# Optimization experiments

Hardware: AMD Instinct MI355X
Metric: run time of the kernel (lower is better)

The kernel has to match this reference:

```python
import jax, jax.numpy as jnp
import numpy as np

N_NODES = 100000
N_EDGES = 1600000
D_IN = 128
D_HID = 64


def setup_inputs() -> dict:
    key = jax.random.key(0)
    k1, k2, k3, k4 = jax.random.split(key, 4)
    x = jax.random.normal(k1, (N_NODES, D_IN), dtype=jnp.float32)
    edge_index = jax.random.randint(k2, (2, N_EDGES), 0, N_NODES, dtype=jnp.int64)
    W1 = jax.random.normal(k3, (D_IN, D_HID), dtype=jnp.float32) / np.sqrt(D_IN)
    b1 = jnp.zeros((D_HID,), dtype=jnp.float32)
    W2 = jax.random.normal(k4, (D_HID, 1), dtype=jnp.float32) / np.sqrt(D_HID)
    b2 = jnp.zeros((1,), dtype=jnp.float32)
    return {"x": x, "edge_index": edge_index, "W1": W1, "b1": b1, "W2": W2, "b2": b2}


def _gcn_layer(x, W, b, src, dst, norm, n):
    # PyG GCNConv: linear transform, then normalized scatter-add aggregation, then bias
    h = x @ W                                   # [N, d_out]
    msg = h[src] * norm[:, None]                # gather + edge-weight   [E', d_out]
    out = jax.ops.segment_sum(msg, dst, num_segments=n)  # scatter-add
    return out + b


def reference(x, edge_index, W1, b1, W2, b2):
    n = x.shape[0]
    loops = jnp.arange(n, dtype=edge_index.dtype)
    src = jnp.concatenate([edge_index[0], loops])  # self-loops added (GCN default)
    dst = jnp.concatenate([edge_index[1], loops])
    # symmetric normalization: deg^{-1/2}[src] * deg^{-1/2}[dst]
    deg = jax.ops.segment_sum(jnp.ones(dst.shape, x.dtype), dst, num_segments=n)
    dis = jnp.where(deg > 0, jax.lax.rsqrt(jnp.maximum(deg, 1e-12)), 0.0)
    norm = dis[src] * dis[dst]
    h = jax.nn.relu(_gcn_layer(x, W1, b1, src, dst, norm, n))
    y = _gcn_layer(h, W2, b2, src, dst, norm, n)   # [N, 1]
    # ConstantPad1d((0, num_node_features-1), 0) -> [N, D_IN]
    return jnp.pad(y, ((0, 0), (0, x.shape[1] - 1)))
```

## Files before the change

### kernel.cpp

```cpp
#include <hip/hip_runtime.h>

#define N_NODES 100000
#define N_EDGES 1600000
#define D_IN 128
#define D_HID 64

#define BKT_SHIFT 8
#define BKT_NODES 256
#define NB 391
#define NBLK 392
#define SLOT 32
#define SEG4 (SLOT / 4)
#define REG4 (NBLK * SEG4)
#define BKT_CAP 5120
#define OVF_CAP 8192

#define FST 512
#define BST 1024
#define GEMM_NB 782

typedef __attribute__((ext_vector_type(8))) short bf16x8;
typedef __attribute__((ext_vector_type(4))) float f32x4;

__device__ __forceinline__ unsigned short f2b(float f) {
    union { float f; unsigned u; } c; c.f = f;
    unsigned r = (c.u + 0x7FFFu + ((c.u >> 16) & 1u)) >> 16;
    return (unsigned short)r;
}
__device__ __forceinline__ float blo(unsigned u) { return __uint_as_float(u << 16); }
__device__ __forceinline__ float bhi(unsigned u) { return __uint_as_float(u & 0xffff0000u); }

#define LS 136
__global__ __launch_bounds__(FST) void k_fused(const int* __restrict__ src,
                                               const int* __restrict__ dst,
                                               int* __restrict__ pairs,
                                               int* __restrict__ cnt_blk,
                                               int* __restrict__ ovf_cnt,
                                               int2* __restrict__ ovf, int E,
                                               const float* __restrict__ x,
                                               const float* __restrict__ W1,
                                               unsigned short* __restrict__ h1s, int n) {
    __shared__ __align__(16) unsigned char smem[52224];
    int tid = threadIdx.x;

    if (blockIdx.x < NBLK) {
        int* lp   = (int*)smem;
        int* lcur = lp + NB * SLOT;
        for (int t = tid; t < NB; t += FST) lcur[t] = 0;
        __syncthreads();
        int chunk = (E + NBLK - 1) / NBLK;
        int beg = blockIdx.x * chunk;
        int end = min(beg + chunk, E);
        for (int e = beg + tid; e < end; e += FST) {
            int d = dst[e], s = src[e];
            int bk = d >> BKT_SHIFT;
            int slot = atomicAdd(&lcur[bk], 1);
            if (slot < SLOT)
                lp[(bk << 5) + slot] = (s << BKT_SHIFT) | (d & (BKT_NODES - 1));
            else {
                int o = atomicAdd(ovf_cnt, 1);
                if (o < OVF_CAP) ovf[o] = make_int2(s, d);
            }
        }
        __syncthreads();
        uint4* p4 = (uint4*)pairs;
        const uint4* lp4 = (const uint4*)lp;
        for (int i4 = tid; i4 < NB * SEG4; i4 += FST) {
            int bk = i4 >> 3;
            int c = min(lcur[bk], SLOT);
            if (((i4 & 7) << 2) < c)
                p4[((size_t)bk * NBLK + blockIdx.x) * SEG4 + (i4 & 7)] = lp4[i4];
        }
        for (int t = tid; t < NB; t += FST)
            cnt_blk[t * NBLK + blockIdx.x] = min(lcur[t], SLOT);
    } else {
        unsigned short* ws = (unsigned short*)smem;
        unsigned short* xs = ws + 64 * LS;
        int half = tid >> 8;
        int t2 = tid & 255;
        int node0 = (blockIdx.x - NBLK) * 128 + half * 64;
        unsigned short* xsh = xs + half * 64 * LS;

#pragma unroll
        for (int it = 0; it < 16; ++it) {
            int e = tid + it * 512;
            int k = e >> 6, f = e & 63;
            ws[f * LS + k] = f2b(W1[e]);
        }
#pragma unroll
        for (int it = 0; it < 8; ++it) {
            int e4 = t2 + it * 256;
            int node = e4 >> 5;
            int k = (e4 & 31) * 4;
            float4 v = make_float4(0.f, 0.f, 0.f, 0.f);
            if (node0 + node < n)
                v = ((const float4*)x)[((size_t)(node0 + node) * D_IN + k) >> 2];
            uint2 u;
            u.x = (unsigned)f2b(v.x) | ((unsigned)f2b(v.y) << 16);
            u.y = (unsigned)f2b(v.z) | ((unsigned)f2b(v.w) << 16);
            *(uint2*)&xsh[node * LS + k] = u;
        }
        __syncthreads();

        int wv = t2 >> 6;
        int lane = t2 & 63;
        int m16 = lane & 15;
        int q = lane >> 4;

        bf16x8 afrag[4];
#pragma unroll
        for (int ks = 0; ks < 4; ++ks)
            afrag[ks] = *(const bf16x8*)&xsh[(wv * 16 + m16) * LS + ks * 32 + q * 8];

        f32x4 acc[4];
#pragma unroll
        for (int ft = 0; ft < 4; ++ft) acc[ft] = (f32x4){0.f, 0.f, 0.f, 0.f};

#pragma unroll
        for (int ft = 0; ft < 4; ++ft)
#pragma unroll
            for (int ks = 0; ks < 4; ++ks) {
                bf16x8 bfrag = *(const bf16x8*)&ws[(ft * 16 + m16) * LS + ks * 32 + q * 8];
                acc[ft] = __builtin_amdgcn_mfma_f32_16x16x32_bf16(afrag[ks], bfrag, acc[ft], 0, 0, 0);
            }

#pragma unroll
        for (int r = 0; r < 4; ++r) {
            int node = node0 + wv * 16 + q * 4 + r;
            if (node < n) {
#pragma unroll
                for (int ft = 0; ft < 4; ++ft)
                    h1s[(size_t)node * D_HID + ft * 16 + m16] = f2b(acc[ft][r]);
            }
        }
    }
}

__global__ __launch_bounds__(BST) void k_bsort(const uint4* __restrict__ pairs4,
                                               const int* __restrict__ cnt_blk,
                                               const int* __restrict__ ovf_cnt,
                                               const int2* __restrict__ ovf,
                                               int* __restrict__ srcs_sorted,
                                               int* __restrict__ row_start,
                                               int* __restrict__ row_end,
                                               float* __restrict__ dis, int n) {
    __shared__ uint4 reg4[REG4];
    __shared__ int segc[NBLK];
    __shared__ int cnt[BKT_NODES];
    __shared__ int exc[BKT_NODES];
    __shared__ int sorted[BKT_CAP];
    __shared__ int nE_sh;
    int b = blockIdx.x;
    int tid = threadIdx.x;
    int node0 = b << BKT_SHIFT;
    int ocnt = min(ovf_cnt[0], OVF_CAP);
    const uint4* region = pairs4 + (size_t)b * REG4;

    for (int i = tid; i < NBLK; i += BST) segc[i] = cnt_blk[b * NBLK + i];
    if (tid < BKT_NODES) cnt[tid] = 0;
    __syncthreads();

    for (int i4 = tid; i4 < REG4; i4 += BST) {
        int c = segc[i4 >> 3];
        int k = (i4 & 7) * 4;
        if (k < c) {
            uint4 v = region[i4];
            reg4[i4] = v;
            atomicAdd(&cnt[v.x & (BKT_NODES - 1)], 1);
            if (k + 1 < c) atomicAdd(&cnt[v.y & (BKT_NODES - 1)], 1);
            if (k + 2 < c) atomicAdd(&cnt[v.z & (BKT_NODES - 1)], 1);
            if (k + 3 < c) atomicAdd(&cnt[v.w & (BKT_NODES - 1)], 1);
        }
    }
    for (int k = tid; k < ocnt; k += BST) {
        int2 e = ovf[k];
        if ((e.y >> BKT_SHIFT) == b) atomicAdd(&cnt[e.y & (BKT_NODES - 1)], 1);
    }
    __syncthreads();

    if (tid < 64) {
        int run = 0;
        for (int c = 0; c < BKT_NODES; c += 64) {
            int v = cnt[c + tid];
            int inc = v;
            for (int off = 1; off < 64; off <<= 1) {
                int t2 = __shfl_up(inc, off);
                if (tid >= off) inc += t2;
            }
            exc[c + tid] = run + inc - v;
            run += __shfl(inc, 63);
        }
        if (tid == 63) nE_sh = run;
    }
    __syncthreads();

    if (tid < BKT_NODES) {
        int node = node0 + tid;
        if (node < n) {
            int rs = b * BKT_CAP + exc[tid];
            row_start[node] = rs;
            row_end[node] = rs + cnt[tid];
            dis[node] = rsqrtf((float)cnt[tid] + 1.0f);
        }
    }
    int nE = nE_sh;
    __syncthreads();
    if (tid < BKT_NODES) cnt[tid] = exc[tid];
    __syncthreads();

    for (int i4 = tid; i4 < REG4; i4 += BST) {
        int c = segc[i4 >> 3];
        int k = (i4 & 7) * 4;
        if (k < c) {
            uint4 v = reg4[i4];
            { int p = atomicAdd(&cnt[v.x & (BKT_NODES - 1)], 1); sorted[p] = (int)(v.x >> 8); }
            if (k + 1 < c) { int p = atomicAdd(&cnt[v.y & (BKT_NODES - 1)], 1); sorted[p] = (int)(v.y >> 8); }
            if (k + 2 < c) { int p = atomicAdd(&cnt[v.z & (BKT_NODES - 1)], 1); sorted[p] = (int)(v.z >> 8); }
            if (k + 3 < c) { int p = atomicAdd(&cnt[v.w & (BKT_NODES - 1)], 1); sorted[p] = (int)(v.w >> 8); }
        }
    }
    for (int k = tid; k < ocnt; k += BST) {
        int2 e = ovf[k];
        if ((e.y >> BKT_SHIFT) == b) {
            int p = atomicAdd(&cnt[e.y & (BKT_NODES - 1)], 1);
            sorted[p] = e.x;
        }
    }
    __syncthreads();

    int gbase = b * BKT_CAP;
    for (int k = tid; k < nE; k += BST)
        srcs_sorted[gbase + k] = sorted[k];
}

__global__ __launch_bounds__(256) void k_gather1(const int* __restrict__ srcs,
                                                 const int* __restrict__ row_start,
                                                 const int* __restrict__ row_end,
                                                 const float* __restrict__ dis,
                                                 const uint4* __restrict__ h4,
                                                 const float* __restrict__ b1,
                                                 const float* __restrict__ W2,
                                                 float* __restrict__ zd, int n) {
    int i = blockIdx.x * 8 + (threadIdx.x >> 5);
    int lane = threadIdx.x & 63;
    int g = (lane >> 3) & 3;
    int m8 = lane & 7;
    float dd = dis[i];

    float a0, a1, a2, a3, a4, a5, a6, a7;
    {
        uint4 u = h4[(unsigned)i * 8u + m8];
        float w = (g == 0) ? dd : 0.f;
        a0 = w * blo(u.x); a1 = w * bhi(u.x);
        a2 = w * blo(u.y); a3 = w * bhi(u.y);
        a4 = w * blo(u.z); a5 = w * bhi(u.z);
        a6 = w * blo(u.w); a7 = w * bhi(u.w);
    }

#define ACC(u, ds) { a0 = fmaf(ds, blo(u.x), a0); a1 = fmaf(ds, bhi(u.x), a1); \
                     a2 = fmaf(ds, blo(u.y), a2); a3 = fmaf(ds, bhi(u.y), a3); \
                     a4 = fmaf(ds, blo(u.z), a4); a5 = fmaf(ds, bhi(u.z), a5); \
                     a6 = fmaf(ds, blo(u.w), a6); a7 = fmaf(ds, bhi(u.w), a7); }
    int end = row_end[i];
    int j = row_start[i] + g;
    for (; j + 12 < end; j += 16) {
        int s0 = srcs[j];
        int s1 = srcs[j + 4];
        int s2 = srcs[j + 8];
        int s3 = srcs[j + 12];
        float d0 = dis[s0], d1 = dis[s1], d2 = dis[s2], d3 = dis[s3];
        uint4 u0 = h4[(unsigned)s0 * 8u + m8];
        uint4 u1 = h4[(unsigned)s1 * 8u + m8];
        uint4 u2 = h4[(unsigned)s2 * 8u + m8];
        uint4 u3 = h4[(unsigned)s3 * 8u + m8];
        ACC(u0, d0); ACC(u1, d1); ACC(u2, d2); ACC(u3, d3);
    }
    for (; j + 4 < end; j += 8) {
        int s0 = srcs[j];
        int s1 = srcs[j + 4];
        float d0 = dis[s0], d1 = dis[s1];
        uint4 u0 = h4[(unsigned)s0 * 8u + m8];
        uint4 u1 = h4[(unsigned)s1 * 8u + m8];
        ACC(u0, d0); ACC(u1, d1);
    }
    if (j < end) {
        int s0 = srcs[j];
        float d0 = dis[s0];
        uint4 u0 = h4[(unsigned)s0 * 8u + m8];
        ACC(u0, d0);
    }
#undef ACC

#pragma unroll
    for (int off = 8; off < 32; off <<= 1) {
        a0 += __shfl_xor(a0, off); a1 += __shfl_xor(a1, off);
        a2 += __shfl_xor(a2, off); a3 += __shfl_xor(a3, off);
        a4 += __shfl_xor(a4, off); a5 += __shfl_xor(a5, off);
        a6 += __shfl_xor(a6, off); a7 += __shfl_xor(a7, off);
    }
    float4 ba = ((const float4*)b1)[m8 * 2];
    float4 bb = ((const float4*)b1)[m8 * 2 + 1];
    float4 wa = ((const float4*)W2)[m8 * 2];
    float4 wb = ((const float4*)W2)[m8 * 2 + 1];
    float v = fmaxf(fmaf(dd, a0, ba.x), 0.f) * wa.x + fmaxf(fmaf(dd, a1, ba.y), 0.f) * wa.y
            + fmaxf(fmaf(dd, a2, ba.z), 0.f) * wa.z + fmaxf(fmaf(dd, a3, ba.w), 0.f) * wa.w
            + fmaxf(fmaf(dd, a4, bb.x), 0.f) * wb.x + fmaxf(fmaf(dd, a5, bb.y), 0.f) * wb.y
            + fmaxf(fmaf(dd, a6, bb.z), 0.f) * wb.z + fmaxf(fmaf(dd, a7, bb.w), 0.f) * wb.w;
#pragma unroll
    for (int off = 1; off < 8; off <<= 1) v += __shfl_xor(v, off);
    if ((lane & 31) == 0) zd[i] = v * dd;
}

__global__ __launch_bounds__(256) void k_gather2(const int* __restrict__ srcs,
                                                 const int* __restrict__ row_start,
                                                 const int* __restrict__ row_end,
                                                 const float* __restrict__ dis,
                                                 const float* __restrict__ zd,
                                                 const float* __restrict__ b2,
                                                 float* __restrict__ out, int n) {
    int i = blockIdx.x * 8 + (threadIdx.x >> 5);
    int l = threadIdx.x & 31;
    float acc = 0.f;
    int beg = row_start[i], end = row_end[i];
    for (int j = beg + l; j < end; j += 32)
        acc += zd[srcs[j]];
#pragma unroll
    for (int off = 1; off < 32; off <<= 1) acc += __shfl_xor(acc, off);
    float y = (acc + zd[i]) * dis[i] + b2[0];
    float4 v = make_float4(0.f, 0.f, 0.f, 0.f);
    if (l == 0) v.x = y;
    ((float4*)out)[(size_t)i * 32 + l] = v;
}

extern "C" void kernel_launch(void* const* d_in, const int* in_sizes, int n_in,
                              void* d_out, int out_size, void* d_ws, size_t ws_size,
                              hipStream_t stream) {
    const float* x  = (const float*)d_in[0];
    const int*   ei = (const int*)d_in[1];
    const float* W1 = (const float*)d_in[2];
    const float* b1 = (const float*)d_in[3];
    const float* W2 = (const float*)d_in[4];
    const float* b2 = (const float*)d_in[5];
    float* out = (float*)d_out;

    const int n = N_NODES;
    const int E = N_EDGES;
    const int* src = ei;
    const int* dst = ei + E;

    int* pairs       = (int*)d_ws;
    int* cnt_blk     = pairs + (size_t)NB * NBLK * SLOT;
    int* srcs_sorted = cnt_blk + (size_t)NB * NBLK;
    int* row_start   = srcs_sorted + (size_t)NB * BKT_CAP;
    int* row_end     = row_start + n;
    int* ovf_cnt     = row_end + n;
    int2* ovf        = (int2*)(ovf_cnt + 4);
    float* dis       = (float*)(ovf + OVF_CAP);
    unsigned short* h1s = (unsigned short*)(dis + n);
    float* zd        = (float*)(h1s + (size_t)n * D_HID);

    hipMemsetAsync(ovf_cnt, 0, sizeof(int), stream);
    k_fused<<<NBLK + GEMM_NB, FST, 0, stream>>>(src, dst, pairs, cnt_blk, ovf_cnt,
                                                ovf, E, x, W1, h1s, n);
    k_bsort<<<NB, BST, 0, stream>>>((const uint4*)pairs, cnt_blk, ovf_cnt, ovf,
                                    srcs_sorted, row_start, row_end, dis, n);
    k_gather1<<<(n + 7) / 8, 256, 0, stream>>>(srcs_sorted, row_start, row_end, dis,
                                               (const uint4*)h1s, b1, W2, zd, n);
    k_gather2<<<(n + 7) / 8, 256, 0, stream>>>(srcs_sorted, row_start, row_end, dis,
                                               zd, b2, out, n);
}
```

Before: 194.0 us.

## Replace two-pass bucket sort CSR build with atomic histogram and scatter

Replaces the per-block LDS bucketing plus per-bucket shared-memory counting sort with a global atomic degree histogram, a per-bucket prefix scan kernel producing row offsets and cursors, and a global-atomic scatter of source ids into CSR order. This removes the large intermediate pairs buffer and overflow path, but relies on millions of global atomics on random addresses and adds one more kernel launch. Edge order within a row becomes nondeterministic, which can change floating-point summation order.

```diff
diff --git a/kernel.cpp b/kernel.cpp
--- a/kernel.cpp
+++ b/kernel.cpp
@@ -8,16 +8,11 @@
 #define BKT_SHIFT 8
 #define BKT_NODES 256
 #define NB 391
-#define NBLK 392
-#define SLOT 32
-#define SEG4 (SLOT / 4)
-#define REG4 (NBLK * SEG4)
 #define BKT_CAP 5120
-#define OVF_CAP 8192
-
+
+#define HIST_NB 392
+#define GEMM_NB 782
 #define FST 512
-#define BST 1024
-#define GEMM_NB 782
 
 typedef __attribute__((ext_vector_type(8))) short bf16x8;
 typedef __attribute__((ext_vector_type(4))) float f32x4;
@@ -31,54 +26,24 @@
 __device__ __forceinline__ float bhi(unsigned u) { return __uint_as_float(u & 0xffff0000u); }
 
 #define LS 136
-__global__ __launch_bounds__(FST) void k_fused(const int* __restrict__ src,
-                                               const int* __restrict__ dst,
-                                               int* __restrict__ pairs,
-                                               int* __restrict__ cnt_blk,
-                                               int* __restrict__ ovf_cnt,
-                                               int2* __restrict__ ovf, int E,
+__global__ __launch_bounds__(FST) void k_fused(const int* __restrict__ dst,
+                                               int* __restrict__ deg, int E,
                                                const float* __restrict__ x,
                                                const float* __restrict__ W1,
                                                unsigned short* __restrict__ h1s, int n) {
     __shared__ __align__(16) unsigned char smem[52224];
     int tid = threadIdx.x;
 
-    if (blockIdx.x < NBLK) {
-        int* lp   = (int*)smem;
-        int* lcur = lp + NB * SLOT;
-        for (int t = tid; t < NB; t += FST) lcur[t] = 0;
-        __syncthreads();
-        int chunk = (E + NBLK - 1) / NBLK;
-        int beg = blockIdx.x * chunk;
-        int end = min(beg + chunk, E);
-        for (int e = beg + tid; e < end; e += FST) {
-            int d = dst[e], s = src[e];
-            int bk = d >> BKT_SHIFT;
-            int slot = atomicAdd(&lcur[bk], 1);
-            if (slot < SLOT)
-                lp[(bk << 5) + slot] = (s << BKT_SHIFT) | (d & (BKT_NODES - 1));
-            else {
-                int o = atomicAdd(ovf_cnt, 1);
-                if (o < OVF_CAP) ovf[o] = make_int2(s, d);
-            }
-        }
-        __syncthreads();
-        uint4* p4 = (uint4*)pairs;
-        const uint4* lp4 = (const uint4*)lp;
-        for (int i4 = tid; i4 < NB * SEG4; i4 += FST) {
-            int bk = i4 >> 3;
-            int c = min(lcur[bk], SLOT);
-            if (((i4 & 7) << 2) < c)
-                p4[((size_t)bk * NBLK + blockIdx.x) * SEG4 + (i4 & 7)] = lp4[i4];
-        }
-        for (int t = tid; t < NB; t += FST)
-            cnt_blk[t * NBLK + blockIdx.x] = min(lcur[t], SLOT);
+    if (blockIdx.x < HIST_NB) {
+        int stride = HIST_NB * FST;
+        for (int e = blockIdx.x * FST + tid; e < E; e += stride)
+            atomicAdd(&deg[dst[e]], 1);
     } else {
         unsigned short* ws = (unsigned short*)smem;
         unsigned short* xs = ws + 64 * LS;
         int half = tid >> 8;
         int t2 = tid & 255;
-        int node0 = (blockIdx.x - NBLK) * 128 + half * 64;
+        int node0 = (blockIdx.x - HIST_NB) * 128 + half * 64;
         unsigned short* xsh = xs + half * 64 * LS;
 
 #pragma unroll
@@ -136,46 +101,18 @@
     }
 }
 
-__global__ __launch_bounds__(BST) void k_bsort(const uint4* __restrict__ pairs4,
-                                               const int* __restrict__ cnt_blk,
-                                               const int* __restrict__ ovf_cnt,
-                                               const int2* __restrict__ ovf,
-                                               int* __restrict__ srcs_sorted,
-                                               int* __restrict__ row_start,
-                                               int* __restrict__ row_end,
-                                               float* __restrict__ dis, int n) {
-    __shared__ uint4 reg4[REG4];
-    __shared__ int segc[NBLK];
+__global__ __launch_bounds__(256) void k_rows(const int* __restrict__ deg,
+                                              int* __restrict__ row_start,
+                                              int* __restrict__ row_end,
+                                              int* __restrict__ cursor,
+                                              float* __restrict__ dis, int n) {
     __shared__ int cnt[BKT_NODES];
     __shared__ int exc[BKT_NODES];
-    __shared__ int sorted[BKT_CAP];
-    __shared__ int nE_sh;
     int b = blockIdx.x;
     int tid = threadIdx.x;
-    int node0 = b << BKT_SHIFT;
-    int ocnt = min(ovf_cnt[0], OVF_CAP);
-    const uint4* region = pairs4 + (size_t)b * REG4;
-
-    for (int i = tid; i < NBLK; i += BST) segc[i] = cnt_blk[b * NBLK + i];
-    if (tid < BKT_NODES) cnt[tid] = 0;
-    __syncthreads();
-
-    for (int i4 = tid; i4 < REG4; i4 += BST) {
-        int c = segc[i4 >> 3];
-        int k = (i4 & 7) * 4;
-        if (k < c) {
-            uint4 v = region[i4];
-            reg4[i4] = v;
-            atomicAdd(&cnt[v.x & (BKT_NODES - 1)], 1);
-            if (k + 1 < c) atomicAdd(&cnt[v.y & (BKT_NODES - 1)], 1);
-            if (k + 2 < c) atomicAdd(&cnt[v.z & (BKT_NODES - 1)], 1);
-            if (k + 3 < c) atomicAdd(&cnt[v.w & (BKT_NODES - 1)], 1);
-        }
-    }
-    for (int k = tid; k < ocnt; k += BST) {
-        int2 e = ovf[k];
-        if ((e.y >> BKT_SHIFT) == b) atomicAdd(&cnt[e.y & (BKT_NODES - 1)], 1);
-    }
+    int node = (b << BKT_SHIFT) + tid;
+    int d = (node < n) ? deg[node] : 0;
+    cnt[tid] = d;
     __syncthreads();
 
     if (tid < 64) {
@@ -190,47 +127,28 @@
             exc[c + tid] = run + inc - v;
             run += __shfl(inc, 63);
         }
-        if (tid == 63) nE_sh = run;
     }
     __syncthreads();
 
-    if (tid < BKT_NODES) {
-        int node = node0 + tid;
-        if (node < n) {
-            int rs = b * BKT_CAP + exc[tid];
-            row_start[node] = rs;
-            row_end[node] = rs + cnt[tid];
-            dis[node] = rsqrtf((float)cnt[tid] + 1.0f);
-        }
-    }
-    int nE = nE_sh;
-    __syncthreads();
-    if (tid < BKT_NODES) cnt[tid] = exc[tid];
-    __syncthreads();
-
-    for (int i4 = tid; i4 < REG4; i4 += BST) {
-        int c = segc[i4 >> 3];
-        int k = (i4 & 7) * 4;
-        if (k < c) {
-            uint4 v = reg4[i4];
-            { int p = atomicAdd(&cnt[v.x & (BKT_NODES - 1)], 1); sorted[p] = (int)(v.x >> 8); }
-            if (k + 1 < c) { int p = atomicAdd(&cnt[v.y & (BKT_NODES - 1)], 1); sorted[p] = (int)(v.y >> 8); }
-            if (k + 2 < c) { int p = atomicAdd(&cnt[v.z & (BKT_NODES - 1)], 1); sorted[p] = (int)(v.z >> 8); }
-            if (k + 3 < c) { int p = atomicAdd(&cnt[v.w & (BKT_NODES - 1)], 1); sorted[p] = (int)(v.w >> 8); }
-        }
-    }
-    for (int k = tid; k < ocnt; k += BST) {
-        int2 e = ovf[k];
-        if ((e.y >> BKT_SHIFT) == b) {
-            int p = atomicAdd(&cnt[e.y & (BKT_NODES - 1)], 1);
-            sorted[p] = e.x;
-        }
-    }
-    __syncthreads();
-
-    int gbase = b * BKT_CAP;
-    for (int k = tid; k < nE; k += BST)
-        srcs_sorted[gbase + k] = sorted[k];
+    if (node < n) {
+        int rs = b * BKT_CAP + exc[tid];
+        row_start[node] = rs;
+        row_end[node] = rs + d;
+        cursor[node] = rs;
+        dis[node] = rsqrtf((float)d + 1.0f);
+    }
+}
+
+__global__ __launch_bounds__(256) void k_scatter(const int* __restrict__ src,
+                                                 const int* __restrict__ dst,
+                                                 int* __restrict__ cursor,
+                                                 int* __restrict__ srcs_sorted, int E) {
+    int stride = gridDim.x * 256;
+    for (int e = blockIdx.x * 256 + threadIdx.x; e < E; e += stride) {
+        int d = dst[e], s = src[e];
+        int p = atomicAdd(&cursor[d], 1);
+        srcs_sorted[p] = s;
+    }
 }
 
 __global__ __launch_bounds__(256) void k_gather1(const int* __restrict__ srcs,
@@ -348,22 +266,19 @@
     const int* src = ei;
     const int* dst = ei + E;
 
-    int* pairs       = (int*)d_ws;
-    int* cnt_blk     = pairs + (size_t)NB * NBLK * SLOT;
-    int* srcs_sorted = cnt_blk + (size_t)NB * NBLK;
+    int* deg         = (int*)d_ws;
+    int* cursor      = deg + n;
+    int* srcs_sorted = cursor + n;
     int* row_start   = srcs_sorted + (size_t)NB * BKT_CAP;
     int* row_end     = row_start + n;
-    int* ovf_cnt     = row_end + n;
-    int2* ovf        = (int2*)(ovf_cnt + 4);
-    float* dis       = (float*)(ovf + OVF_CAP);
+    float* dis       = (float*)(row_end + n);
     unsigned short* h1s = (unsigned short*)(dis + n);
     float* zd        = (float*)(h1s + (size_t)n * D_HID);
 
-    hipMemsetAsync(ovf_cnt, 0, sizeof(int), stream);
-    k_fused<<<NBLK + GEMM_NB, FST, 0, stream>>>(src, dst, pairs, cnt_blk, ovf_cnt,
-                                                ovf, E, x, W1, h1s, n);
-    k_bsort<<<NB, BST, 0, stream>>>((const uint4*)pairs, cnt_blk, ovf_cnt, ovf,
-                                    srcs_sorted, row_start, row_end, dis, n);
+    hipMemsetAsync(deg, 0, n * sizeof(int), stream);
+    k_fused<<<HIST_NB + GEMM_NB, FST, 0, stream>>>(dst, deg, E, x, W1, h1s, n);
+    k_rows<<<NB, 256, 0, stream>>>(deg, row_start, row_end, cursor, dis, n);
+    k_scatter<<<1568, 256, 0, stream>>>(src, dst, cursor, srcs_sorted, E);
     k_gather1<<<(n + 7) / 8, 256, 0, stream>>>(srcs_sorted, row_start, row_end, dis,
                                                (const uint4*)h1s, b1, W2, zd, n);
     k_gather2<<<(n + 7) / 8, 256, 0, stream>>>(srcs_sorted, row_start, row_end, dis,
```

Measured after the change: 348.6 us. 1.8x slower.

## Quantize hidden features to int8 with per-node scales for gather

Applied to the files above, without the earlier changes.

The GEMM epilogue now quantizes each node's 64-wide hidden row to int8, using a per-node absmax scale. It stages the rows through shared memory for coalesced 16-byte stores. The sort kernel folds the degree normalization and the quantization scale into one per-node factor. The first gather then reads 8-byte int8 rows instead of 16-byte bf16 rows, which halves the random-gather traffic. In exchange it loses precision relative to bf16 and adds a shuffle reduction and a block sync in the GEMM epilogue.

```diff
diff --git a/kernel.cpp b/kernel.cpp
--- a/kernel.cpp
+++ b/kernel.cpp
@@ -39,7 +39,8 @@
                                                int2* __restrict__ ovf, int E,
                                                const float* __restrict__ x,
                                                const float* __restrict__ W1,
-                                               unsigned short* __restrict__ h1s, int n) {
+                                               unsigned char* __restrict__ h1s8,
+                                               float* __restrict__ scale, int n) {
     __shared__ __align__(16) unsigned char smem[52224];
     int tid = threadIdx.x;
 
@@ -124,14 +125,31 @@
                 acc[ft] = __builtin_amdgcn_mfma_f32_16x16x32_bf16(afrag[ks], bfrag, acc[ft], 0, 0, 0);
             }
 
+        char* hs8 = (char*)xsh;
 #pragma unroll
         for (int r = 0; r < 4; ++r) {
-            int node = node0 + wv * 16 + q * 4 + r;
-            if (node < n) {
-#pragma unroll
-                for (int ft = 0; ft < 4; ++ft)
-                    h1s[(size_t)node * D_HID + ft * 16 + m16] = f2b(acc[ft][r]);
+            int nl = wv * 16 + q * 4 + r;
+            int node = node0 + nl;
+            float mv = fmaxf(fmaxf(fabsf(acc[0][r]), fabsf(acc[1][r])),
+                             fmaxf(fabsf(acc[2][r]), fabsf(acc[3][r])));
+#pragma unroll
+            for (int off = 1; off < 16; off <<= 1) mv = fmaxf(mv, __shfl_xor(mv, off));
+            float inv = (mv > 0.f) ? 127.0f / mv : 0.f;
+            if (m16 == 0 && node < n) scale[node] = mv * (1.0f / 127.0f);
+#pragma unroll
+            for (int ft = 0; ft < 4; ++ft) {
+                int qi = __float2int_rn(acc[ft][r] * inv);
+                qi = max(-127, min(127, qi));
+                hs8[nl * 64 + ft * 16 + m16] = (char)qi;
             }
+        }
+        __syncthreads();
+        const uint4* hs4 = (const uint4*)hs8;
+        uint4* h84 = (uint4*)h1s8;
+        {
+            int nl = t2 >> 2;
+            int node = node0 + nl;
+            if (node < n) h84[(size_t)node * 4 + (t2 & 3)] = hs4[t2];
         }
     }
 }
@@ -140,10 +158,12 @@
                                                const int* __restrict__ cnt_blk,
                                                const int* __restrict__ ovf_cnt,
                                                const int2* __restrict__ ovf,
+                                               const float* __restrict__ scale,
                                                int* __restrict__ srcs_sorted,
                                                int* __restrict__ row_start,
                                                int* __restrict__ row_end,
-                                               float* __restrict__ dis, int n) {
+                                               float* __restrict__ dis,
+                                               float* __restrict__ dq, int n) {
     __shared__ uint4 reg4[REG4];
     __shared__ int segc[NBLK];
     __shared__ int cnt[BKT_NODES];
@@ -200,7 +220,9 @@
             int rs = b * BKT_CAP + exc[tid];
             row_start[node] = rs;
             row_end[node] = rs + cnt[tid];
-            dis[node] = rsqrtf((float)cnt[tid] + 1.0f);
+            float dv = rsqrtf((float)cnt[tid] + 1.0f);
+            dis[node] = dv;
+            dq[node] = dv * scale[node];
         }
     }
     int nE = nE_sh;
@@ -237,7 +259,8 @@
                                                  const int* __restrict__ row_start,
                                                  const int* __restrict__ row_end,
                                                  const float* __restrict__ dis,
-                                                 const uint4* __restrict__ h4,
+                                                 const float* __restrict__ dq,
+                                                 const uint2* __restrict__ h2,
                                                  const float* __restrict__ b1,
                                                  const float* __restrict__ W2,
                                                  float* __restrict__ zd, int n) {
@@ -249,18 +272,27 @@
 
     float a0, a1, a2, a3, a4, a5, a6, a7;
     {
-        uint4 u = h4[(unsigned)i * 8u + m8];
-        float w = (g == 0) ? dd : 0.f;
-        a0 = w * blo(u.x); a1 = w * bhi(u.x);
-        a2 = w * blo(u.y); a3 = w * bhi(u.y);
-        a4 = w * blo(u.z); a5 = w * bhi(u.z);
-        a6 = w * blo(u.w); a7 = w * bhi(u.w);
-    }
-
-#define ACC(u, ds) { a0 = fmaf(ds, blo(u.x), a0); a1 = fmaf(ds, bhi(u.x), a1); \
-                     a2 = fmaf(ds, blo(u.y), a2); a3 = fmaf(ds, bhi(u.y), a3); \
-                     a4 = fmaf(ds, blo(u.z), a4); a5 = fmaf(ds, bhi(u.z), a5); \
-                     a6 = fmaf(ds, blo(u.w), a6); a7 = fmaf(ds, bhi(u.w), a7); }
+        uint2 u = h2[(unsigned)i * 8u + m8];
+        float w = (g == 0) ? dq[i] : 0.f;
+        a0 = w * (float)((int)(u.x << 24) >> 24);
+        a1 = w * (float)((int)(u.x << 16) >> 24);
+        a2 = w * (float)((int)(u.x << 8) >> 24);
+        a3 = w * (float)((int)u.x >> 24);
+        a4 = w * (float)((int)(u.y << 24) >> 24);
+        a5 = w * (float)((int)(u.y << 16) >> 24);
+        a6 = w * (float)((int)(u.y << 8) >> 24);
+        a7 = w * (float)((int)u.y >> 24);
+    }
+
+#define ACC8(u, ds) { \
+    a0 = fmaf(ds, (float)((int)(u.x << 24) >> 24), a0); \
+    a1 = fmaf(ds, (float)((int)(u.x << 16) >> 24), a1); \
+    a2 = fmaf(ds, (float)((int)(u.x << 8) >> 24), a2);  \
+    a3 = fmaf(ds, (float)((int)u.x >> 24), a3);         \
+    a4 = fmaf(ds, (float)((int)(u.y << 24) >> 24), a4); \
+    a5 = fmaf(ds, (float)((int)(u.y << 16) >> 24), a5); \
+    a6 = fmaf(ds, (float)((int)(u.y << 8) >> 24), a6);  \
+    a7 = fmaf(ds, (float)((int)u.y >> 24), a7); }
     int end = row_end[i];
     int j = row_start[i] + g;
     for (; j + 12 < end; j += 16) {
@@ -268,28 +300,28 @@
         int s1 = srcs[j + 4];
         int s2 = srcs[j + 8];
         int s3 = srcs[j + 12];
-        float d0 = dis[s0], d1 = dis[s1], d2 = dis[s2], d3 = dis[s3];
-        uint4 u0 = h4[(unsigned)s0 * 8u + m8];
-        uint4 u1 = h4[(unsigned)s1 * 8u + m8];
-        uint4 u2 = h4[(unsigned)s2 * 8u + m8];
-        uint4 u3 = h4[(unsigned)s3 * 8u + m8];
-        ACC(u0, d0); ACC(u1, d1); ACC(u2, d2); ACC(u3, d3);
+        float d0 = dq[s0], d1 = dq[s1], d2 = dq[s2], d3 = dq[s3];
+        uint2 u0 = h2[(unsigned)s0 * 8u + m8];
+        uint2 u1 = h2[(unsigned)s1 * 8u + m8];
+        uint2 u2 = h2[(unsigned)s2 * 8u + m8];
+        uint2 u3 = h2[(unsigned)s3 * 8u + m8];
+        ACC8(u0, d0); ACC8(u1, d1); ACC8(u2, d2); ACC8(u3, d3);
     }
     for (; j + 4 < end; j += 8) {
         int s0 = srcs[j];
         int s1 = srcs[j + 4];
-        float d0 = dis[s0], d1 = dis[s1];
-        uint4 u0 = h4[(unsigned)s0 * 8u + m8];
-        uint4 u1 = h4[(unsigned)s1 * 8u + m8];
-        ACC(u0, d0); ACC(u1, d1);
+        float d0 = dq[s0], d1 = dq[s1];
+        uint2 u0 = h2[(unsigned)s0 * 8u + m8];
+        uint2 u1 = h2[(unsigned)s1 * 8u + m8];
+        ACC8(u0, d0); ACC8(u1, d1);
     }
     if (j < end) {
         int s0 = srcs[j];
-        float d0 = dis[s0];
-        uint4 u0 = h4[(unsigned)s0 * 8u + m8];
-        ACC(u0, d0);
-    }
-#undef ACC
+        float d0 = dq[s0];
+        uint2 u0 = h2[(unsigned)s0 * 8u + m8];
+        ACC8(u0, d0);
+    }
+#undef ACC8
 
 #pragma unroll
     for (int off = 8; off < 32; off <<= 1) {
@@ -348,7 +380,8 @@
     const int* src = ei;
     const int* dst = ei + E;
 
-    int* pairs       = (int*)d_ws;
+    unsigned char* h1s8 = (unsigned char*)d_ws;
+    int* pairs       = (int*)(h1s8 + (size_t)n * D_HID);
     int* cnt_blk     = pairs + (size_t)NB * NBLK * SLOT;
     int* srcs_sorted = cnt_blk + (size_t)NB * NBLK;
     int* row_start   = srcs_sorted + (size_t)NB * BKT_CAP;
@@ -356,16 +389,17 @@
     int* ovf_cnt     = row_end + n;
     int2* ovf        = (int2*)(ovf_cnt + 4);
     float* dis       = (float*)(ovf + OVF_CAP);
-    unsigned short* h1s = (unsigned short*)(dis + n);
-    float* zd        = (float*)(h1s + (size_t)n * D_HID);
+    float* scale     = dis + n;
+    float* dq        = scale + n;
+    float* zd        = dq + n;
 
     hipMemsetAsync(ovf_cnt, 0, sizeof(int), stream);
     k_fused<<<NBLK + GEMM_NB, FST, 0, stream>>>(src, dst, pairs, cnt_blk, ovf_cnt,
-                                                ovf, E, x, W1, h1s, n);
-    k_bsort<<<NB, BST, 0, stream>>>((const uint4*)pairs, cnt_blk, ovf_cnt, ovf,
-                                    srcs_sorted, row_start, row_end, dis, n);
-    k_gather1<<<(n + 7) / 8, 256, 0, stream>>>(srcs_sorted, row_start, row_end, dis,
-                                               (const uint4*)h1s, b1, W2, zd, n);
+                                                ovf, E, x, W1, h1s8, scale, n);
+    k_bsort<<<NB, BST, 0, stream>>>((const uint4*)pairs, cnt_blk, ovf_cnt, ovf, scale,
+                                    srcs_sorted, row_start, row_end, dis, dq, n);
+    k_gather1<<<(n + 7) / 8, 256, 0, stream>>>(srcs_sorted, row_start, row_end, dis, dq,
+                                               (const uint2*)h1s8, b1, W2, zd, n);
     k_gather2<<<(n + 7) / 8, 256, 0, stream>>>(srcs_sorted, row_start, row_end, dis,
                                                zd, b2, out, n);
 }
```

After: 176.8 us. -8.8%, faster.
